# Kernel optimization log

Measured on AMD Instinct MI355X. Metric: run time of the kernel, lower is better.

Reference implementation:

```python
import jax, jax.numpy as jnp
import numpy as np

NUM_CLASSES = 4096
K_INIT = 3
NUM_CENTROIDS = NUM_CLASSES * K_INIT  # 12288
N, D = 16384, 1024
TEMPERATURE = 1.0


def setup_inputs() -> dict:
    key = jax.random.key(0)
    k1, k2, k3 = jax.random.split(key, 3)
    X = jax.random.normal(k1, (N, D), dtype=jnp.float32)
    centroids = jax.random.normal(k2, (NUM_CENTROIDS, D), dtype=jnp.float32)
    centroid_labels = jax.random.randint(k3, (NUM_CENTROIDS,), 0, NUM_CLASSES)
    return {"X": X, "centroids": centroids, "centroid_labels": centroid_labels}


def reference(X, centroids, centroid_labels):
    # _cdist with distance='cosine': similarity is a plain matmul X @ C.T -> [N, K]
    sim = jnp.matmul(X, centroids.T)
    # soft assignment, soft_type='softmax' with temperature scaling over all centroids
    assign = jax.nn.softmax(sim / TEMPERATURE, axis=-1)  # [N, K]
    # aggregate centroid assignment mass per class via centroid_labels
    # segment_sum over K axis: [K, N] -> [NUM_CLASSES, N] -> [N, NUM_CLASSES]
    class_scores = jax.ops.segment_sum(assign.T, centroid_labels, num_segments=NUM_CLASSES).T
    return class_scores
```

## Files before the change

### kernel.cpp

```cpp
#include <hip/hip_runtime.h>
#include <hip/hip_fp16.h>

#define AS1 __attribute__((address_space(1)))
#define AS3 __attribute__((address_space(3)))

typedef _Float16 f16x8 __attribute__((ext_vector_type(8)));
typedef float f32x4 __attribute__((ext_vector_type(4)));

constexpr int NROWS = 16384;
constexpr int DIM   = 1024;
constexpr int KCENT = 12288;
constexpr int NCLS  = 4096;
constexpr int BM = 128, BN = 128, BK = 32;
constexpr int KSTEPS = DIM / BK;
constexpr int STATS_T = KCENT / 64;

__launch_bounds__(256)
__global__ void build_perm(const int* __restrict__ lab, int* __restrict__ iperm,
                           ushort* __restrict__ segstart) {
  __shared__ ushort slab[KCENT];
  __shared__ unsigned scnt[NCLS];
  __shared__ unsigned sstart[NCLS + 1];
  __shared__ unsigned redw[4];
  const int tid = threadIdx.x;
  const int lane = tid & 63, wv = tid >> 6;

  for (int i = tid; i < KCENT; i += 256) slab[i] = (ushort)lab[i];
  for (int i = tid; i < NCLS; i += 256) scnt[i] = 0u;
  __syncthreads();
  for (int i = tid; i < KCENT; i += 256) atomicAdd(&scnt[slab[i]], 1u);
  __syncthreads();

  unsigned loc = 0;
#pragma unroll
  for (int j = 0; j < 16; ++j) loc += scnt[tid * 16 + j];
  unsigned sc = loc;
#pragma unroll
  for (int off = 1; off < 64; off <<= 1) {
    unsigned v = __shfl_up(sc, off, 64);
    if (lane >= off) sc += v;
  }
  if (lane == 63) redw[wv] = sc;
  __syncthreads();
  unsigned wbase = 0;
  for (int w = 0; w < wv; ++w) wbase += redw[w];
  unsigned run = wbase + sc - loc;
#pragma unroll
  for (int j = 0; j < 16; ++j) {
    sstart[tid * 16 + j] = run;
    run += scnt[tid * 16 + j];
  }
  if (tid == 255) sstart[NCLS] = run;
  __syncthreads();

  for (int i = tid; i < NCLS; i += 256) scnt[i] = sstart[i];
  __syncthreads();
  for (int i = tid; i < KCENT; i += 256) {
    unsigned pos = atomicAdd(&scnt[slab[i]], 1u);
    iperm[pos] = i;
  }
  __syncthreads();
  for (int c = tid; c < NCLS; c += 256) {
    int a = (int)sstart[c], b = (int)sstart[c + 1];
    for (int i = a + 1; i < b; ++i) {
      int v = iperm[i], j = i - 1;
      while (j >= a && iperm[j] > v) { iperm[j + 1] = iperm[j]; --j; }
      iperm[j + 1] = v;
    }
  }
  for (int i = tid; i <= NCLS; i += 256) segstart[i] = (ushort)sstart[i];
}

__global__ void convert_f16(const float4* __restrict__ src, ushort4* __restrict__ dst, int n4) {
  int i = blockIdx.x * blockDim.x + threadIdx.x;
  if (i >= n4) return;
  float4 v = src[i];
  float a[4] = {v.x, v.y, v.z, v.w};
  unsigned short hs[4];
#pragma unroll
  for (int j = 0; j < 4; ++j) hs[j] = __builtin_bit_cast(unsigned short, (_Float16)a[j]);
  dst[i] = make_ushort4(hs[0], hs[1], hs[2], hs[3]);
}

__launch_bounds__(256)
__global__ void convert_perm_f16(const float4* __restrict__ src, const int* __restrict__ iperm,
                                 ushort4* __restrict__ dst) {
  const int p = blockIdx.x;
  const int srow = iperm[p];
  const int t = threadIdx.x;
  float4 v = src[(size_t)srow * (DIM / 4) + t];
  unsigned short hs[4];
  float a[4] = {v.x, v.y, v.z, v.w};
#pragma unroll
  for (int j = 0; j < 4; ++j) hs[j] = __builtin_bit_cast(unsigned short, (_Float16)a[j]);
  dst[(size_t)p * (DIM / 4) + t] = make_ushort4(hs[0], hs[1], hs[2], hs[3]);
}

__launch_bounds__(256, 4)
__global__ void gemm_softmax(const _Float16* __restrict__ Xf, const _Float16* __restrict__ Cf,
                             _Float16* __restrict__ expo, float2* __restrict__ stats,
                             int row0) {
  __shared__ _Float16 sA[BM * BK], sB[BM * BK];
  const int tid  = threadIdx.x;
  const int lane = tid & 63;
  const int wv   = tid >> 6;
  const int wr   = wv >> 1, wc = wv & 1;
  const int bm = blockIdx.x, bn = blockIdx.y;
  const size_t arow0 = (size_t)row0 + (size_t)bm * BM;
  const size_t brow0 = (size_t)bn * BN;
  const int lbase = bm * BM;

  f32x4 acc[4][4] = {};

  const int srow = lane >> 2;
  const int scol = (((lane & 3) ^ ((lane >> 3) & 3)) * 8);

  for (int ks = 0; ks < KSTEPS; ++ks) {
    __syncthreads();
    const int kcol = ks * BK;
#pragma unroll
    for (int s = 0; s < 2; ++s) {
      const int iss = wv * 2 + s;
      const int r = iss * 16 + srow;
      const size_t ga = (arow0 + (size_t)r) * DIM + kcol + scol;
      const size_t gb = (brow0 + (size_t)r) * DIM + kcol + scol;
      const int lo_off = iss * 512;
      __builtin_amdgcn_global_load_lds((const AS1 void*)(Xf + ga), (AS3 void*)(sA + lo_off), 16, 0, 0);
      __builtin_amdgcn_global_load_lds((const AS1 void*)(Cf + gb), (AS3 void*)(sB + lo_off), 16, 0, 0);
    }
    __syncthreads();

    f16x8 af[4], bf[4];
    const int kk = (((lane >> 4) ^ ((lane >> 1) & 3)) * 8);
    const int rsel = lane & 15;
#pragma unroll
    for (int m = 0; m < 4; ++m) {
      const int ar = wr * 64 + m * 16 + rsel;
      af[m] = *(const f16x8*)(sA + ar * BK + kk);
      const int br = wc * 64 + m * 16 + rsel;
      bf[m] = *(const f16x8*)(sB + br * BK + kk);
    }
#pragma unroll
    for (int m = 0; m < 4; ++m)
#pragma unroll
      for (int n = 0; n < 4; ++n)
        acc[m][n] = __builtin_amdgcn_mfma_f32_16x16x32_f16(af[m], bf[n], acc[m][n], 0, 0, 0);
  }

  const int g  = lane >> 4;
  const int cl = lane & 15;
  const int tileIdx = bn * 2 + wc;
#pragma unroll
  for (int m = 0; m < 4; ++m) {
#pragma unroll
    for (int j = 0; j < 4; ++j) {
      const int lrow = lbase + wr * 64 + m * 16 + g * 4 + j;
      float v0 = acc[m][0][j], v1 = acc[m][1][j], v2 = acc[m][2][j], v3 = acc[m][3][j];
      float mx = fmaxf(fmaxf(v0, v1), fmaxf(v2, v3));
#pragma unroll
      for (int s2 = 1; s2 < 16; s2 <<= 1) mx = fmaxf(mx, __shfl_xor(mx, s2, 64));
      float p0 = __expf(v0 - mx), p1 = __expf(v1 - mx), p2 = __expf(v2 - mx), p3 = __expf(v3 - mx);
      float sm = p0 + p1 + p2 + p3;
#pragma unroll
      for (int s2 = 1; s2 < 16; s2 <<= 1) sm += __shfl_xor(sm, s2, 64);
      _Float16* ep = expo + (size_t)lrow * KCENT + brow0 + wc * 64;
      ep[ 0 + cl] = (_Float16)p0;
      ep[16 + cl] = (_Float16)p1;
      ep[32 + cl] = (_Float16)p2;
      ep[48 + cl] = (_Float16)p3;
      if (cl == 0) stats[(size_t)lrow * STATS_T + tileIdx] = make_float2(mx, sm);
    }
  }
}

__launch_bounds__(256)
__global__ void scatter_classes(const _Float16* __restrict__ expo, const float2* __restrict__ stats,
                                const ushort* __restrict__ segstart, float* __restrict__ out,
                                int row0) {
  __shared__ __align__(16) _Float16 srow[KCENT];
  __shared__ __align__(16) float souts[NCLS];
  __shared__ ushort ss[NCLS + 1];
  __shared__ float cf[STATS_T];
  __shared__ float red[8];
  const int row = blockIdx.x;
  const int tid = threadIdx.x;
  const int lane = tid & 63, wv = tid >> 6;

  const uint4* ep8 = (const uint4*)(expo + (size_t)row * KCENT);
  uint4* sr8 = (uint4*)srow;
#pragma unroll
  for (int i = 0; i < 6; ++i) sr8[i * 256 + tid] = ep8[i * 256 + tid];
  for (int i = tid; i <= NCLS; i += 256) ss[i] = segstart[i];

  float mt = -3.4e38f, zt = 0.f;
  if (tid < STATS_T) {
    float2 s0 = stats[(size_t)row * STATS_T + tid];
    mt = s0.x; zt = s0.y;
  }
  float m = mt;
#pragma unroll
  for (int s2 = 1; s2 < 64; s2 <<= 1) m = fmaxf(m, __shfl_xor(m, s2, 64));
  if (lane == 0) red[wv] = m;
  __syncthreads();
  m = fmaxf(fmaxf(red[0], red[1]), fmaxf(red[2], red[3]));
  float e = (tid < STATS_T) ? __expf(mt - m) : 0.f;
  float z = zt * e;
#pragma unroll
  for (int s2 = 1; s2 < 64; s2 <<= 1) z += __shfl_xor(z, s2, 64);
  if (lane == 0) red[4 + wv] = z;
  __syncthreads();
  z = (red[4] + red[5]) + (red[6] + red[7]);
  if (tid < STATS_T) cf[tid] = e / z;
  __syncthreads();

#pragma unroll
  for (int j = 0; j < 16; ++j) {
    const int c = tid + j * 256;
    const int a = ss[c], b = ss[c + 1];
    float s = 0.f;
    for (int k = a; k < b; ++k) s += (float)srow[k] * cf[k >> 6];
    souts[c] = s;
  }
  __syncthreads();

  float4* orow = (float4*)(out + (size_t)(row0 + row) * NCLS);
  const float4* o4 = (const float4*)souts;
#pragma unroll
  for (int i = 0; i < 4; ++i) orow[i * 256 + tid] = o4[i * 256 + tid];
}

extern "C" void kernel_launch(void* const* d_in, const int* in_sizes, int n_in,
                              void* d_out, int out_size, void* d_ws, size_t ws_size,
                              hipStream_t stream) {
  (void)in_sizes; (void)n_in; (void)out_size;
  const float* X = (const float*)d_in[0];
  const float* C = (const float*)d_in[1];
  const int* labels = (const int*)d_in[2];
  float* out = (float*)d_out;

  char* ws = (char*)d_ws;
  size_t off = 0;
  auto carve = [&](size_t bytes) -> char* {
    char* p = ws + off;
    off += (bytes + 255) & ~(size_t)255;
    return p;
  };
  _Float16* Xf = (_Float16*)carve((size_t)NROWS * DIM * 2);
  _Float16* Cf = (_Float16*)carve((size_t)KCENT * DIM * 2);
  int* iperm = (int*)carve((size_t)KCENT * 4);
  ushort* segstart = (ushort*)carve((size_t)(NCLS + 1) * 2);
  const size_t fixed = off;

  const size_t per_row = (size_t)KCENT * 2 + (size_t)STATS_T * 8;
  size_t avail = (ws_size > fixed + 4096) ? (ws_size - fixed - 4096) : 0;
  long Rmax = (long)(avail / per_row);
  Rmax = (Rmax / 128) * 128;
  if (Rmax < 128) Rmax = 128;
  if (Rmax > NROWS) Rmax = NROWS;
  _Float16* expo = (_Float16*)carve((size_t)Rmax * KCENT * 2);
  float2* stats  = (float2*)carve((size_t)Rmax * STATS_T * 8);

  build_perm<<<1, 256, 0, stream>>>(labels, iperm, segstart);
  {
    int n4x = NROWS * DIM / 4;
    convert_f16<<<(n4x + 255) / 256, 256, 0, stream>>>((const float4*)X, (ushort4*)Xf, n4x);
    convert_perm_f16<<<KCENT, 256, 0, stream>>>((const float4*)C, iperm, (ushort4*)Cf);
  }

  for (int r0 = 0; r0 < NROWS; r0 += (int)Rmax) {
    int R = (NROWS - r0 < (int)Rmax) ? (NROWS - r0) : (int)Rmax;
    dim3 grid(R / BM, KCENT / BN);
    gemm_softmax<<<grid, 256, 0, stream>>>(Xf, Cf, expo, stats, r0);
    scatter_classes<<<R, 256, 0, stream>>>(expo, stats, segstart, out, r0);
  }
}
```

Measured before the change: 1.180 ms.

## Replace per-class segment loop with per-element class ids and run-length reduction

Changes the class aggregation from per-class segment loops over shared memory to per-thread contiguous chunks of 48 sorted centroids. Each chunk is loaded into registers along with a precomputed per-element class id array, then reduced by run-length grouping. A neighbour-merge step joins classes that span chunk boundaries. This removes load imbalance from variable segment lengths and the shared staging of the row, at the cost of a larger per-element label read and a merge step that assumes no class spans more than two chunks.

```diff
diff --git a/kernel.cpp b/kernel.cpp
--- a/kernel.cpp
+++ b/kernel.cpp
@@ -17,7 +17,7 @@
 
 __launch_bounds__(256)
 __global__ void build_perm(const int* __restrict__ lab, int* __restrict__ iperm,
-                           ushort* __restrict__ segstart) {
+                           ushort* __restrict__ elemclass) {
   __shared__ ushort slab[KCENT];
   __shared__ unsigned scnt[NCLS];
   __shared__ unsigned sstart[NCLS + 1];
@@ -68,7 +68,10 @@
       iperm[j + 1] = v;
     }
   }
-  for (int i = tid; i <= NCLS; i += 256) segstart[i] = (ushort)sstart[i];
+  for (int c = tid; c < NCLS; c += 256) {
+    int a = (int)sstart[c], b = (int)sstart[c + 1];
+    for (int i = a; i < b; ++i) elemclass[i] = (ushort)c;
+  }
 }
 
 __global__ void convert_f16(const float4* __restrict__ src, ushort4* __restrict__ dst, int n4) {
@@ -175,22 +178,32 @@
 
 __launch_bounds__(256)
 __global__ void scatter_classes(const _Float16* __restrict__ expo, const float2* __restrict__ stats,
-                                const ushort* __restrict__ segstart, float* __restrict__ out,
+                                const ushort* __restrict__ elemclass, float* __restrict__ out,
                                 int row0) {
-  __shared__ __align__(16) _Float16 srow[KCENT];
   __shared__ __align__(16) float souts[NCLS];
-  __shared__ ushort ss[NCLS + 1];
   __shared__ float cf[STATS_T];
   __shared__ float red[8];
+  __shared__ int   sBC[512];
+  __shared__ float sBP[512];
   const int row = blockIdx.x;
   const int tid = threadIdx.x;
   const int lane = tid & 63, wv = tid >> 6;
 
   const uint4* ep8 = (const uint4*)(expo + (size_t)row * KCENT);
-  uint4* sr8 = (uint4*)srow;
-#pragma unroll
-  for (int i = 0; i < 6; ++i) sr8[i * 256 + tid] = ep8[i * 256 + tid];
-  for (int i = tid; i <= NCLS; i += 256) ss[i] = segstart[i];
+  const uint4* ec8 = (const uint4*)elemclass;
+  unsigned ew[24], lw[24];
+#pragma unroll
+  for (int i = 0; i < 6; ++i) {
+    uint4 v = ep8[6 * tid + i];
+    ew[4 * i] = v.x; ew[4 * i + 1] = v.y; ew[4 * i + 2] = v.z; ew[4 * i + 3] = v.w;
+  }
+#pragma unroll
+  for (int i = 0; i < 6; ++i) {
+    uint4 u = ec8[6 * tid + i];
+    lw[4 * i] = u.x; lw[4 * i + 1] = u.y; lw[4 * i + 2] = u.z; lw[4 * i + 3] = u.w;
+  }
+
+  for (int i = tid; i < NCLS; i += 256) souts[i] = 0.f;
 
   float mt = -3.4e38f, zt = 0.f;
   if (tid < STATS_T) {
@@ -213,13 +226,42 @@
   if (tid < STATS_T) cf[tid] = e / z;
   __syncthreads();
 
-#pragma unroll
-  for (int j = 0; j < 16; ++j) {
-    const int c = tid + j * 256;
-    const int a = ss[c], b = ss[c + 1];
-    float s = 0.f;
-    for (int k = a; k < b; ++k) s += (float)srow[k] * cf[k >> 6];
-    souts[c] = s;
+  const int kbase = 48 * tid;
+  const int t0 = kbase >> 6;
+  const float cfA = cf[t0];
+  const float cfB = cf[(t0 + 1 < STATS_T) ? t0 + 1 : t0];
+  const int isw = 64 - (kbase & 63);
+
+  int cur = -1; float run2 = 0.f;
+  int leadc = -1; float leadp = 0.f; bool first = true;
+#pragma unroll
+  for (int i = 0; i < 48; ++i) {
+    const unsigned w = ew[i >> 1];
+    const unsigned short eh = (unsigned short)((i & 1) ? (w >> 16) : (w & 0xffffu));
+    const unsigned lwv = lw[i >> 1];
+    const int c = (int)((i & 1) ? (lwv >> 16) : (lwv & 0xffffu));
+    const float p = (float)__builtin_bit_cast(_Float16, eh) * ((i < isw) ? cfA : cfB);
+    if (c != cur) {
+      if (cur >= 0) {
+        if (first) { leadc = cur; leadp = run2; first = false; }
+        else souts[cur] = run2;
+      }
+      cur = c; run2 = 0.f;
+    }
+    run2 += p;
+  }
+  if (first) leadc = -1;
+  sBC[tid] = leadc;       sBP[tid] = leadp;
+  sBC[256 + tid] = cur;   sBP[256 + tid] = run2;
+  __syncthreads();
+
+  {
+    const int c1 = sBC[256 + tid];
+    float s = sBP[256 + tid];
+    if (tid < 255 && sBC[tid + 1] == c1) s += sBP[tid + 1];
+    souts[c1] = s;
+    const int c0 = sBC[tid];
+    if (c0 >= 0 && (tid == 0 || sBC[256 + tid - 1] != c0)) souts[c0] = sBP[tid];
   }
   __syncthreads();
 
@@ -248,7 +290,7 @@
   _Float16* Xf = (_Float16*)carve((size_t)NROWS * DIM * 2);
   _Float16* Cf = (_Float16*)carve((size_t)KCENT * DIM * 2);
   int* iperm = (int*)carve((size_t)KCENT * 4);
-  ushort* segstart = (ushort*)carve((size_t)(NCLS + 1) * 2);
+  ushort* elemclass = (ushort*)carve((size_t)KCENT * 2);
   const size_t fixed = off;
 
   const size_t per_row = (size_t)KCENT * 2 + (size_t)STATS_T * 8;
@@ -260,7 +302,7 @@
   _Float16* expo = (_Float16*)carve((size_t)Rmax * KCENT * 2);
   float2* stats  = (float2*)carve((size_t)Rmax * STATS_T * 8);
 
-  build_perm<<<1, 256, 0, stream>>>(labels, iperm, segstart);
+  build_perm<<<1, 256, 0, stream>>>(labels, iperm, elemclass);
   {
     int n4x = NROWS * DIM / 4;
     convert_f16<<<(n4x + 255) / 256, 256, 0, stream>>>((const float4*)X, (ushort4*)Xf, n4x);
@@ -271,6 +313,6 @@
     int R = (NROWS - r0 < (int)Rmax) ? (NROWS - r0) : (int)Rmax;
     dim3 grid(R / BM, KCENT / BN);
     gemm_softmax<<<grid, 256, 0, stream>>>(Xf, Cf, expo, stats, r0);
-    scatter_classes<<<R, 256, 0, stream>>>(expo, stats, segstart, out, r0);
-  }
-}
+    scatter_classes<<<R, 256, 0, stream>>>(expo, stats, elemclass, out, r0);
+  }
+}
```

Measured after the change: 1.026 ms. -13.1%, faster.
